# Kernel optimization log

Measured on AMD Instinct MI355X. Metric: run time of the kernel, lower is better.

The kernel has to match this reference:

```python
import jax, jax.numpy as jnp
import numpy as np

H1, H2 = 32, 16


def _gru_layer(x, W_ih, W_hh, b_ih, b_hh, H):
    # x: [B, T, I]; W_ih: [3H, I]; W_hh: [3H, H]; biases: [3H]
    # PyTorch gate order: r, z, n
    B = x.shape[0]
    xW = jnp.einsum('bti,gi->btg', x, W_ih) + b_ih  # [B, T, 3H]

    def step(h, xw_t):
        gh = h @ W_hh.T + b_hh                      # [B, 3H]
        r = jax.nn.sigmoid(xw_t[:, :H] + gh[:, :H])
        z = jax.nn.sigmoid(xw_t[:, H:2 * H] + gh[:, H:2 * H])
        n = jnp.tanh(xw_t[:, 2 * H:] + r * gh[:, 2 * H:])
        h_new = (1.0 - z) * n + z * h
        return h_new, h_new

    h0 = jnp.zeros((B, H), dtype=x.dtype)
    _, ys = jax.lax.scan(step, h0, jnp.swapaxes(xW, 0, 1))  # ys: [T, B, H]
    return jnp.swapaxes(ys, 0, 1)


def setup_inputs() -> dict:
    key = jax.random.key(0)
    ks = jax.random.split(key, 11)
    B, I, T, O = 4096, 8, 512, 1

    def u(k, shape, fan):
        s = 1.0 / np.sqrt(fan)
        return jax.random.uniform(k, shape, jnp.float32, -s, s)

    return {
        'input_seq': jax.random.normal(ks[0], (B, I, T), jnp.float32),
        'W_ih1': u(ks[1], (3 * H1, I), H1),
        'W_hh1': u(ks[2], (3 * H1, H1), H1),
        'b_ih1': u(ks[3], (3 * H1,), H1),
        'b_hh1': u(ks[4], (3 * H1,), H1),
        'W_ih2': u(ks[5], (3 * H2, H1), H2),
        'W_hh2': u(ks[6], (3 * H2, H2), H2),
        'b_ih2': u(ks[7], (3 * H2,), H2),
        'b_hh2': u(ks[8], (3 * H2,), H2),
        'W_lin': u(ks[9], (O, H2), H2),
        'b_lin': u(ks[10], (O,), H2),
    }


def reference(input_seq, W_ih1, W_hh1, b_ih1, b_hh1,
              W_ih2, W_hh2, b_ih2, b_hh2, W_lin, b_lin):
    x = jnp.transpose(input_seq, (0, 2, 1))          # [B, T, I]
    h1 = _gru_layer(x, W_ih1, W_hh1, b_ih1, b_hh1, H1)   # [B, T, 32]
    h2 = _gru_layer(h1, W_ih2, W_hh2, b_ih2, b_hh2, H2)  # [B, T, 16]
    out = h2[:, -1, :] @ W_lin.T + b_lin             # [B, O]
    return jnp.squeeze(out)                          # [B] when O == 1
```

## Files before the change

### kernel.cpp

```cpp
#include <hip/hip_runtime.h>

typedef __attribute__((ext_vector_type(4))) float    f32x4;
typedef __attribute__((ext_vector_type(4))) unsigned u32x4;
typedef __attribute__((ext_vector_type(8))) short    s16x8;

#define LOG2E 1.44269504088896340736f
__device__ __forceinline__ float fexp2(float x){ return __builtin_amdgcn_exp2f(x); }
__device__ __forceinline__ float frcp (float x){ return __builtin_amdgcn_rcpf(x); }
__device__ __forceinline__ float sigf (float x){ return frcp(1.0f + fexp2(-LOG2E*x)); }
__device__ __forceinline__ float tanh_(float x){ return 1.0f - 2.0f*frcp(1.0f + fexp2(2.0f*LOG2E*x)); }

__device__ __forceinline__ f32x4 mfma16(u32x4 a, u32x4 b, f32x4 c){
    return __builtin_amdgcn_mfma_f32_16x16x32_bf16(
        __builtin_bit_cast(s16x8, a), __builtin_bit_cast(s16x8, b), c, 0, 0, 0);
}

__device__ __forceinline__ unsigned rne_bf16(float f){
    unsigned u = __builtin_bit_cast(unsigned, f);
    return (u + 0x7fffu + ((u >> 16) & 1u)) >> 16;
}
__device__ __forceinline__ u32x4 packdup4(const float* p){
    u32x4 r;
    #pragma unroll
    for (int q = 0; q < 4; ++q) {
        unsigned w = rne_bf16(p[q]);
        r[q] = w | (w << 16);
    }
    return r;
}
__device__ __forceinline__ u32x4 packdup4_lo(const float* p){
    u32x4 r;
    #pragma unroll
    for (int q = 0; q < 4; ++q) {
        unsigned wh = rne_bf16(p[q]);
        float    wf = __builtin_bit_cast(float, wh << 16);
        unsigned wl = rne_bf16(p[q] - wf);
        r[q] = wl | (wl << 16);
    }
    return r;
}
__device__ __forceinline__ unsigned packsplit(float h){
    unsigned hu = __builtin_bit_cast(unsigned, h);
    unsigned hm = hu & 0xffff0000u;
    float rem = h - __builtin_bit_cast(float, hm);
    unsigned ru = __builtin_bit_cast(unsigned, rem);
    return (hm >> 16) | (ru & 0xffff0000u);
}

__global__ __launch_bounds__(192)
void gru2_mfma(const float* __restrict__ x_g,
               const float* __restrict__ Wih1, const float* __restrict__ Whh1,
               const float* __restrict__ bih1, const float* __restrict__ bhh1,
               const float* __restrict__ Wih2, const float* __restrict__ Whh2,
               const float* __restrict__ bih2, const float* __restrict__ bhh2,
               const float* __restrict__ Wlin, const float* __restrict__ blin,
               float* __restrict__ out)
{
    const int tid = threadIdx.x;
    const int wid = tid / 64;
    const int l   = tid & 63;
    const int sl  = l & 15;
    const int g   = l >> 4;
    const int b0  = blockIdx.x * 16;

    __shared__ unsigned xpk[32][16][12];
    __shared__ unsigned h1b[2][16][36];
    __shared__ unsigned zl[4];

    {
        unsigned* p1 = &h1b[0][0][0];
        for (int k = tid; k < 2*16*36; k += 192) p1[k] = 0u;
        if (tid < 4) zl[tid] = 0u;
    }

    u32x4 fR0,fR0l, fR1,fR1l, fR2,fR2l, fZ0,fZ0l, fZ1,fZ1l, fZ2,fZ2l,
          fX0,fX0l, fA,fAl, fB,fBl;
    f32x4 cbR, cbZ, cbX, cbH;
    const u32x4 zero4 = {0u,0u,0u,0u};

    if (wid < 2) {
        const int Ub = wid * 16;
        const int gr = Ub + sl, gz = 32 + Ub + sl, gn = 64 + Ub + sl;
        fR0  = (g < 2) ? packdup4   (Wih1 + gr*8 + 4*g) : zero4;
        fR0l = (g < 2) ? packdup4_lo(Wih1 + gr*8 + 4*g) : zero4;
        fR1  = packdup4   (Whh1 + gr*32 + 4*g);
        fR1l = packdup4_lo(Whh1 + gr*32 + 4*g);
        fR2  = packdup4   (Whh1 + gr*32 + 16 + 4*g);
        fR2l = packdup4_lo(Whh1 + gr*32 + 16 + 4*g);
        fZ0  = (g < 2) ? packdup4   (Wih1 + gz*8 + 4*g) : zero4;
        fZ0l = (g < 2) ? packdup4_lo(Wih1 + gz*8 + 4*g) : zero4;
        fZ1  = packdup4   (Whh1 + gz*32 + 4*g);
        fZ1l = packdup4_lo(Whh1 + gz*32 + 4*g);
        fZ2  = packdup4   (Whh1 + gz*32 + 16 + 4*g);
        fZ2l = packdup4_lo(Whh1 + gz*32 + 16 + 4*g);
        fX0  = (g < 2) ? packdup4   (Wih1 + gn*8 + 4*g) : zero4;
        fX0l = (g < 2) ? packdup4_lo(Wih1 + gn*8 + 4*g) : zero4;
        fA   = packdup4   (Whh1 + gn*32 + 4*g);
        fAl  = packdup4_lo(Whh1 + gn*32 + 4*g);
        fB   = packdup4   (Whh1 + gn*32 + 16 + 4*g);
        fBl  = packdup4_lo(Whh1 + gn*32 + 16 + 4*g);
        #pragma unroll
        for (int e = 0; e < 4; ++e) {
            const int u = Ub + 4*g + e;
            cbR[e] = bih1[u]      + bhh1[u];
            cbZ[e] = bih1[32+u]   + bhh1[32+u];
            cbX[e] = bih1[64+u];
            cbH[e] = bhh1[64+u];
        }
    } else {
        fR0  = packdup4   (Wih2 + sl*32 + 4*g);
        fR0l = packdup4_lo(Wih2 + sl*32 + 4*g);
        fR1  = packdup4   (Wih2 + sl*32 + 16 + 4*g);
        fR1l = packdup4_lo(Wih2 + sl*32 + 16 + 4*g);
        fR2  = packdup4   (Whh2 + sl*16 + 4*g);
        fR2l = packdup4_lo(Whh2 + sl*16 + 4*g);
        fZ0  = packdup4   (Wih2 + (16+sl)*32 + 4*g);
        fZ0l = packdup4_lo(Wih2 + (16+sl)*32 + 4*g);
        fZ1  = packdup4   (Wih2 + (16+sl)*32 + 16 + 4*g);
        fZ1l = packdup4_lo(Wih2 + (16+sl)*32 + 16 + 4*g);
        fZ2  = packdup4   (Whh2 + (16+sl)*16 + 4*g);
        fZ2l = packdup4_lo(Whh2 + (16+sl)*16 + 4*g);
        fX0  = packdup4   (Wih2 + (32+sl)*32 + 4*g);
        fX0l = packdup4_lo(Wih2 + (32+sl)*32 + 4*g);
        fA   = packdup4   (Wih2 + (32+sl)*32 + 16 + 4*g);
        fAl  = packdup4_lo(Wih2 + (32+sl)*32 + 16 + 4*g);
        fB   = packdup4   (Whh2 + (32+sl)*16 + 4*g);
        fBl  = packdup4_lo(Whh2 + (32+sl)*16 + 4*g);
        #pragma unroll
        for (int e = 0; e < 4; ++e) {
            const int u = 4*g + e;
            cbR[e] = bih2[u]    + bhh2[u];
            cbZ[e] = bih2[16+u] + bhh2[16+u];
            cbX[e] = bih2[32+u];
            cbH[e] = bhh2[32+u];
        }
    }

    float hv[4] = {0.f,0.f,0.f,0.f};
    u32x4 own   = {0u,0u,0u,0u};
    const f32x4 zc = {0.f,0.f,0.f,0.f};

    #pragma unroll 1
    for (int i = 0; i <= 512; ++i) {
        if ((i & 31) == 0 && i < 512) {
            if (tid < 128) {
                const int s  = tid >> 3;
                const int ii = tid & 7;
                const float* xg = x_g + ((size_t)(b0 + s))*4096 + ii*512 + i;
                #pragma unroll
                for (int w4 = 0; w4 < 8; ++w4) {
                    const f32x4 v = *(const f32x4*)(xg + 4*w4);
                    #pragma unroll
                    for (int e = 0; e < 4; ++e)
                        xpk[w4*4 + e][s][ii] = packsplit(v[e]);
                }
            }
            __syncthreads();
        }

        const int pr = (i + 1) & 1;

        if (wid < 2 && i < 512) {
            const int tt = i & 31;
            const u32x4 bT0 = (g < 2) ? *(const u32x4*)&xpk[tt][sl][4*g]
                                      : *(const u32x4*)&zl[0];
            u32x4 bT1, bT2;
            if (wid == 0) { bT1 = own;
                            bT2 = *(const u32x4*)&h1b[pr][sl][16 + 4*g]; }
            else          { bT1 = *(const u32x4*)&h1b[pr][sl][4*g];
                            bT2 = own; }
            f32x4 crh, crl, czh, czl, cx, cnh, cnl;
            crh = mfma16(fR0,  bT0, cbR); crh = mfma16(fR1,  bT1, crh); crh = mfma16(fR2,  bT2, crh);
            crl = mfma16(fR0l, bT0, zc ); crl = mfma16(fR1l, bT1, crl); crl = mfma16(fR2l, bT2, crl);
            czh = mfma16(fZ0,  bT0, cbZ); czh = mfma16(fZ1,  bT1, czh); czh = mfma16(fZ2,  bT2, czh);
            czl = mfma16(fZ0l, bT0, zc ); czl = mfma16(fZ1l, bT1, czl); czl = mfma16(fZ2l, bT2, czl);
            cx  = mfma16(fX0,  bT0, cbX); cx  = mfma16(fX0l, bT0, cx );
            cnh = mfma16(fA,   bT1, cbH); cnh = mfma16(fB,   bT2, cnh);
            cnl = mfma16(fAl,  bT1, zc ); cnl = mfma16(fBl,  bT2, cnl);
            #pragma unroll
            for (int e = 0; e < 4; ++e) {
                const float r = sigf(crh[e] + crl[e]);
                const float z = sigf(czh[e] + czl[e]);
                const float n = tanh_(fmaf(r, cnh[e] + cnl[e], cx[e]));
                const float h = n + z*(hv[e] - n);
                hv[e] = h;
                own[e] = packsplit(h);
            }
            *(u32x4*)&h1b[i & 1][sl][(wid ? 16 : 0) + 4*g] = own;
        }

        if (wid == 2 && i > 0) {
            const u32x4 bU0 = *(const u32x4*)&h1b[pr][sl][4*g];
            const u32x4 bU1 = *(const u32x4*)&h1b[pr][sl][16 + 4*g];
            const u32x4 bU2 = own;
            f32x4 crh, crl, czh, czl, cx, cn;
            crh = mfma16(fR0,  bU0, cbR); crh = mfma16(fR1,  bU1, crh); crh = mfma16(fR2,  bU2, crh);
            crl = mfma16(fR0l, bU0, zc ); crl = mfma16(fR1l, bU1, crl); crl = mfma16(fR2l, bU2, crl);
            czh = mfma16(fZ0,  bU0, cbZ); czh = mfma16(fZ1,  bU1, czh); czh = mfma16(fZ2,  bU2, czh);
            czl = mfma16(fZ0l, bU0, zc ); czl = mfma16(fZ1l, bU1, czl); czl = mfma16(fZ2l, bU2, czl);
            cx  = mfma16(fX0,  bU0, cbX); cx  = mfma16(fA,   bU1, cx );
            cx  = mfma16(fX0l, bU0, cx ); cx  = mfma16(fAl,  bU1, cx );
            cn  = mfma16(fB,   bU2, cbH); cn  = mfma16(fBl,  bU2, cn );
            #pragma unroll
            for (int e = 0; e < 4; ++e) {
                const float r = sigf(crh[e] + crl[e]);
                const float z = sigf(czh[e] + czl[e]);
                const float n = tanh_(fmaf(r, cn[e], cx[e]));
                const float h = n + z*(hv[e] - n);
                hv[e] = h;
                own[e] = packsplit(h);
            }
        }

        __syncthreads();
    }

    if (wid == 2) {
        float acc = 0.0f;
        acc = fmaf(Wlin[4*g+0], hv[0], acc);
        acc = fmaf(Wlin[4*g+1], hv[1], acc);
        acc = fmaf(Wlin[4*g+2], hv[2], acc);
        acc = fmaf(Wlin[4*g+3], hv[3], acc);
        acc += __shfl_xor(acc, 16, 64);
        acc += __shfl_xor(acc, 32, 64);
        if (g == 0) out[b0 + sl] = acc + blin[0];
    }
}

extern "C" void kernel_launch(void* const* d_in, const int* in_sizes, int n_in,
                              void* d_out, int out_size, void* d_ws, size_t ws_size,
                              hipStream_t stream) {
    const float* x    = (const float*)d_in[0];
    const float* Wih1 = (const float*)d_in[1];
    const float* Whh1 = (const float*)d_in[2];
    const float* bih1 = (const float*)d_in[3];
    const float* bhh1 = (const float*)d_in[4];
    const float* Wih2 = (const float*)d_in[5];
    const float* Whh2 = (const float*)d_in[6];
    const float* bih2 = (const float*)d_in[7];
    const float* bhh2 = (const float*)d_in[8];
    const float* Wlin = (const float*)d_in[9];
    const float* blin = (const float*)d_in[10];
    float* out = (float*)d_out;

    dim3 grid(256), block(192);
    hipLaunchKernelGGL(gru2_mfma, grid, block, 0, stream,
                       x, Wih1, Whh1, bih1, bhh1, Wih2, Whh2, bih2, bhh2,
                       Wlin, blin, out);
}
```

Measured before the change: 311.6 us.

## Merge both GRU layers into a single wavefront and drop block barriers

The block shrinks from three wavefronts (two for layer 1, one for layer 2) to one wavefront that computes both layer-1 halves and then layer 2 each timestep. All weight fragments stay in registers, the hidden state is passed in registers, the h1 ping-pong LDS buffer goes away, and the per-step __syncthreads are removed. The next timestep's x fragment is also prefetched from LDS one step ahead. In exchange, all MFMAs run on one SIMD, so layer 2 now follows layer 1 serially inside each step instead of being pipelined across waves, and register pressure rises sharply.

```diff
diff --git a/kernel.cpp b/kernel.cpp
--- a/kernel.cpp
+++ b/kernel.cpp
@@ -22,10 +22,7 @@
 __device__ __forceinline__ u32x4 packdup4(const float* p){
     u32x4 r;
     #pragma unroll
-    for (int q = 0; q < 4; ++q) {
-        unsigned w = rne_bf16(p[q]);
-        r[q] = w | (w << 16);
-    }
+    for (int q = 0; q < 4; ++q) { unsigned w = rne_bf16(p[q]); r[q] = w | (w << 16); }
     return r;
 }
 __device__ __forceinline__ u32x4 packdup4_lo(const float* p){
@@ -47,7 +44,7 @@
     return (hm >> 16) | (ru & 0xffff0000u);
 }
 
-__global__ __launch_bounds__(192)
+__global__ __launch_bounds__(64, 1)
 void gru2_mfma(const float* __restrict__ x_g,
                const float* __restrict__ Wih1, const float* __restrict__ Whh1,
                const float* __restrict__ bih1, const float* __restrict__ bhh1,
@@ -56,171 +53,179 @@
                const float* __restrict__ Wlin, const float* __restrict__ blin,
                float* __restrict__ out)
 {
-    const int tid = threadIdx.x;
-    const int wid = tid / 64;
-    const int l   = tid & 63;
-    const int sl  = l & 15;
-    const int g   = l >> 4;
-    const int b0  = blockIdx.x * 16;
+    const int l  = threadIdx.x;
+    const int sl = l & 15;
+    const int g  = l >> 4;
+    const int b0 = blockIdx.x * 16;
 
     __shared__ unsigned xpk[32][16][12];
-    __shared__ unsigned h1b[2][16][36];
-    __shared__ unsigned zl[4];
-
-    {
-        unsigned* p1 = &h1b[0][0][0];
-        for (int k = tid; k < 2*16*36; k += 192) p1[k] = 0u;
-        if (tid < 4) zl[tid] = 0u;
-    }
-
-    u32x4 fR0,fR0l, fR1,fR1l, fR2,fR2l, fZ0,fZ0l, fZ1,fZ1l, fZ2,fZ2l,
-          fX0,fX0l, fA,fAl, fB,fBl;
-    f32x4 cbR, cbZ, cbX, cbH;
+
     const u32x4 zero4 = {0u,0u,0u,0u};
-
-    if (wid < 2) {
-        const int Ub = wid * 16;
+    const f32x4 zc    = {0.f,0.f,0.f,0.f};
+
+    u32x4 f1[2][18];
+    f32x4 cb1[2][4];
+    #pragma unroll
+    for (int hf = 0; hf < 2; ++hf) {
+        const int Ub = hf * 16;
         const int gr = Ub + sl, gz = 32 + Ub + sl, gn = 64 + Ub + sl;
-        fR0  = (g < 2) ? packdup4   (Wih1 + gr*8 + 4*g) : zero4;
-        fR0l = (g < 2) ? packdup4_lo(Wih1 + gr*8 + 4*g) : zero4;
-        fR1  = packdup4   (Whh1 + gr*32 + 4*g);
-        fR1l = packdup4_lo(Whh1 + gr*32 + 4*g);
-        fR2  = packdup4   (Whh1 + gr*32 + 16 + 4*g);
-        fR2l = packdup4_lo(Whh1 + gr*32 + 16 + 4*g);
-        fZ0  = (g < 2) ? packdup4   (Wih1 + gz*8 + 4*g) : zero4;
-        fZ0l = (g < 2) ? packdup4_lo(Wih1 + gz*8 + 4*g) : zero4;
-        fZ1  = packdup4   (Whh1 + gz*32 + 4*g);
-        fZ1l = packdup4_lo(Whh1 + gz*32 + 4*g);
-        fZ2  = packdup4   (Whh1 + gz*32 + 16 + 4*g);
-        fZ2l = packdup4_lo(Whh1 + gz*32 + 16 + 4*g);
-        fX0  = (g < 2) ? packdup4   (Wih1 + gn*8 + 4*g) : zero4;
-        fX0l = (g < 2) ? packdup4_lo(Wih1 + gn*8 + 4*g) : zero4;
-        fA   = packdup4   (Whh1 + gn*32 + 4*g);
-        fAl  = packdup4_lo(Whh1 + gn*32 + 4*g);
-        fB   = packdup4   (Whh1 + gn*32 + 16 + 4*g);
-        fBl  = packdup4_lo(Whh1 + gn*32 + 16 + 4*g);
+        f1[hf][0]  = (g < 2) ? packdup4   (Wih1 + gr*8 + 4*g) : zero4;
+        f1[hf][1]  = (g < 2) ? packdup4_lo(Wih1 + gr*8 + 4*g) : zero4;
+        f1[hf][2]  = packdup4   (Whh1 + gr*32 + 4*g);
+        f1[hf][3]  = packdup4_lo(Whh1 + gr*32 + 4*g);
+        f1[hf][4]  = packdup4   (Whh1 + gr*32 + 16 + 4*g);
+        f1[hf][5]  = packdup4_lo(Whh1 + gr*32 + 16 + 4*g);
+        f1[hf][6]  = (g < 2) ? packdup4   (Wih1 + gz*8 + 4*g) : zero4;
+        f1[hf][7]  = (g < 2) ? packdup4_lo(Wih1 + gz*8 + 4*g) : zero4;
+        f1[hf][8]  = packdup4   (Whh1 + gz*32 + 4*g);
+        f1[hf][9]  = packdup4_lo(Whh1 + gz*32 + 4*g);
+        f1[hf][10] = packdup4   (Whh1 + gz*32 + 16 + 4*g);
+        f1[hf][11] = packdup4_lo(Whh1 + gz*32 + 16 + 4*g);
+        f1[hf][12] = (g < 2) ? packdup4   (Wih1 + gn*8 + 4*g) : zero4;
+        f1[hf][13] = (g < 2) ? packdup4_lo(Wih1 + gn*8 + 4*g) : zero4;
+        f1[hf][14] = packdup4   (Whh1 + gn*32 + 4*g);
+        f1[hf][15] = packdup4_lo(Whh1 + gn*32 + 4*g);
+        f1[hf][16] = packdup4   (Whh1 + gn*32 + 16 + 4*g);
+        f1[hf][17] = packdup4_lo(Whh1 + gn*32 + 16 + 4*g);
         #pragma unroll
         for (int e = 0; e < 4; ++e) {
             const int u = Ub + 4*g + e;
-            cbR[e] = bih1[u]      + bhh1[u];
-            cbZ[e] = bih1[32+u]   + bhh1[32+u];
-            cbX[e] = bih1[64+u];
-            cbH[e] = bhh1[64+u];
-        }
-    } else {
-        fR0  = packdup4   (Wih2 + sl*32 + 4*g);
-        fR0l = packdup4_lo(Wih2 + sl*32 + 4*g);
-        fR1  = packdup4   (Wih2 + sl*32 + 16 + 4*g);
-        fR1l = packdup4_lo(Wih2 + sl*32 + 16 + 4*g);
-        fR2  = packdup4   (Whh2 + sl*16 + 4*g);
-        fR2l = packdup4_lo(Whh2 + sl*16 + 4*g);
-        fZ0  = packdup4   (Wih2 + (16+sl)*32 + 4*g);
-        fZ0l = packdup4_lo(Wih2 + (16+sl)*32 + 4*g);
-        fZ1  = packdup4   (Wih2 + (16+sl)*32 + 16 + 4*g);
-        fZ1l = packdup4_lo(Wih2 + (16+sl)*32 + 16 + 4*g);
-        fZ2  = packdup4   (Whh2 + (16+sl)*16 + 4*g);
-        fZ2l = packdup4_lo(Whh2 + (16+sl)*16 + 4*g);
-        fX0  = packdup4   (Wih2 + (32+sl)*32 + 4*g);
-        fX0l = packdup4_lo(Wih2 + (32+sl)*32 + 4*g);
-        fA   = packdup4   (Wih2 + (32+sl)*32 + 16 + 4*g);
-        fAl  = packdup4_lo(Wih2 + (32+sl)*32 + 16 + 4*g);
-        fB   = packdup4   (Whh2 + (32+sl)*16 + 4*g);
-        fBl  = packdup4_lo(Whh2 + (32+sl)*16 + 4*g);
+            cb1[hf][0][e] = bih1[u]      + bhh1[u];
+            cb1[hf][1][e] = bih1[32+u]   + bhh1[32+u];
+            cb1[hf][2][e] = bih1[64+u];
+            cb1[hf][3][e] = bhh1[64+u];
+        }
+    }
+    u32x4 f2[18];
+    f32x4 cb2[4];
+    {
+        f2[0]  = packdup4   (Wih2 + sl*32 + 4*g);
+        f2[1]  = packdup4_lo(Wih2 + sl*32 + 4*g);
+        f2[2]  = packdup4   (Wih2 + sl*32 + 16 + 4*g);
+        f2[3]  = packdup4_lo(Wih2 + sl*32 + 16 + 4*g);
+        f2[4]  = packdup4   (Whh2 + sl*16 + 4*g);
+        f2[5]  = packdup4_lo(Whh2 + sl*16 + 4*g);
+        f2[6]  = packdup4   (Wih2 + (16+sl)*32 + 4*g);
+        f2[7]  = packdup4_lo(Wih2 + (16+sl)*32 + 4*g);
+        f2[8]  = packdup4   (Wih2 + (16+sl)*32 + 16 + 4*g);
+        f2[9]  = packdup4_lo(Wih2 + (16+sl)*32 + 16 + 4*g);
+        f2[10] = packdup4   (Whh2 + (16+sl)*16 + 4*g);
+        f2[11] = packdup4_lo(Whh2 + (16+sl)*16 + 4*g);
+        f2[12] = packdup4   (Wih2 + (32+sl)*32 + 4*g);
+        f2[13] = packdup4_lo(Wih2 + (32+sl)*32 + 4*g);
+        f2[14] = packdup4   (Wih2 + (32+sl)*32 + 16 + 4*g);
+        f2[15] = packdup4_lo(Wih2 + (32+sl)*32 + 16 + 4*g);
+        f2[16] = packdup4   (Whh2 + (32+sl)*16 + 4*g);
+        f2[17] = packdup4_lo(Whh2 + (32+sl)*16 + 4*g);
         #pragma unroll
         for (int e = 0; e < 4; ++e) {
             const int u = 4*g + e;
-            cbR[e] = bih2[u]    + bhh2[u];
-            cbZ[e] = bih2[16+u] + bhh2[16+u];
-            cbX[e] = bih2[32+u];
-            cbH[e] = bhh2[32+u];
-        }
-    }
-
-    float hv[4] = {0.f,0.f,0.f,0.f};
-    u32x4 own   = {0u,0u,0u,0u};
-    const f32x4 zc = {0.f,0.f,0.f,0.f};
+            cb2[0][e] = bih2[u]    + bhh2[u];
+            cb2[1][e] = bih2[16+u] + bhh2[16+u];
+            cb2[2][e] = bih2[32+u];
+            cb2[3][e] = bhh2[32+u];
+        }
+    }
+
+    float hv1[2][4] = {{0.f,0.f,0.f,0.f},{0.f,0.f,0.f,0.f}};
+    float hv2[4]    = {0.f,0.f,0.f,0.f};
+    u32x4 own1_0 = zero4, own1_1 = zero4, own2 = zero4;
+    u32x4 xnext  = zero4;
 
     #pragma unroll 1
-    for (int i = 0; i <= 512; ++i) {
-        if ((i & 31) == 0 && i < 512) {
-            if (tid < 128) {
-                const int s  = tid >> 3;
-                const int ii = tid & 7;
-                const float* xg = x_g + ((size_t)(b0 + s))*4096 + ii*512 + i;
+    for (int i = 0; i < 512; ++i) {
+        const int tt = i & 31;
+        if (tt == 0) {
+            #pragma unroll
+            for (int r = 0; r < 2; ++r) {
+                const int ii = 2*g + r;
+                const float* xg = x_g + (size_t)(b0 + sl)*4096 + ii*512 + i;
                 #pragma unroll
                 for (int w4 = 0; w4 < 8; ++w4) {
                     const f32x4 v = *(const f32x4*)(xg + 4*w4);
                     #pragma unroll
                     for (int e = 0; e < 4; ++e)
-                        xpk[w4*4 + e][s][ii] = packsplit(v[e]);
+                        xpk[w4*4 + e][sl][ii] = packsplit(v[e]);
                 }
             }
-            __syncthreads();
-        }
-
-        const int pr = (i + 1) & 1;
-
-        if (wid < 2 && i < 512) {
-            const int tt = i & 31;
-            const u32x4 bT0 = (g < 2) ? *(const u32x4*)&xpk[tt][sl][4*g]
-                                      : *(const u32x4*)&zl[0];
-            u32x4 bT1, bT2;
-            if (wid == 0) { bT1 = own;
-                            bT2 = *(const u32x4*)&h1b[pr][sl][16 + 4*g]; }
-            else          { bT1 = *(const u32x4*)&h1b[pr][sl][4*g];
-                            bT2 = own; }
-            f32x4 crh, crl, czh, czl, cx, cnh, cnl;
-            crh = mfma16(fR0,  bT0, cbR); crh = mfma16(fR1,  bT1, crh); crh = mfma16(fR2,  bT2, crh);
-            crl = mfma16(fR0l, bT0, zc ); crl = mfma16(fR1l, bT1, crl); crl = mfma16(fR2l, bT2, crl);
-            czh = mfma16(fZ0,  bT0, cbZ); czh = mfma16(fZ1,  bT1, czh); czh = mfma16(fZ2,  bT2, czh);
-            czl = mfma16(fZ0l, bT0, zc ); czl = mfma16(fZ1l, bT1, czl); czl = mfma16(fZ2l, bT2, czl);
-            cx  = mfma16(fX0,  bT0, cbX); cx  = mfma16(fX0l, bT0, cx );
-            cnh = mfma16(fA,   bT1, cbH); cnh = mfma16(fB,   bT2, cnh);
-            cnl = mfma16(fAl,  bT1, zc ); cnl = mfma16(fBl,  bT2, cnl);
+            if (g < 2) xnext = *(const u32x4*)&xpk[0][sl][4*g];
+        }
+        const u32x4 bT0 = xnext;
+        if (g < 2 && tt < 31) xnext = *(const u32x4*)&xpk[tt+1][sl][4*g];
+
+        f32x4 acc[2][7];
+        #pragma unroll
+        for (int hf = 0; hf < 2; ++hf) {
+            f32x4 crh = mfma16(f1[hf][2],  own1_0, cb1[hf][0]);
+            crh       = mfma16(f1[hf][4],  own1_1, crh);
+            crh       = mfma16(f1[hf][0],  bT0,    crh);
+            f32x4 crl = mfma16(f1[hf][3],  own1_0, zc);
+            crl       = mfma16(f1[hf][5],  own1_1, crl);
+            crl       = mfma16(f1[hf][1],  bT0,    crl);
+            f32x4 czh = mfma16(f1[hf][8],  own1_0, cb1[hf][1]);
+            czh       = mfma16(f1[hf][10], own1_1, czh);
+            czh       = mfma16(f1[hf][6],  bT0,    czh);
+            f32x4 czl = mfma16(f1[hf][9],  own1_0, zc);
+            czl       = mfma16(f1[hf][11], own1_1, czl);
+            czl       = mfma16(f1[hf][7],  bT0,    czl);
+            f32x4 cx  = mfma16(f1[hf][12], bT0,    cb1[hf][2]);
+            cx        = mfma16(f1[hf][13], bT0,    cx);
+            f32x4 cnh = mfma16(f1[hf][14], own1_0, cb1[hf][3]);
+            cnh       = mfma16(f1[hf][16], own1_1, cnh);
+            f32x4 cnl = mfma16(f1[hf][15], own1_0, zc);
+            cnl       = mfma16(f1[hf][17], own1_1, cnl);
+            acc[hf][0]=crh; acc[hf][1]=crl; acc[hf][2]=czh; acc[hf][3]=czl;
+            acc[hf][4]=cx;  acc[hf][5]=cnh; acc[hf][6]=cnl;
+        }
+        #pragma unroll
+        for (int hf = 0; hf < 2; ++hf) {
+            u32x4 ow;
             #pragma unroll
             for (int e = 0; e < 4; ++e) {
-                const float r = sigf(crh[e] + crl[e]);
-                const float z = sigf(czh[e] + czl[e]);
-                const float n = tanh_(fmaf(r, cnh[e] + cnl[e], cx[e]));
-                const float h = n + z*(hv[e] - n);
-                hv[e] = h;
-                own[e] = packsplit(h);
+                const float r = sigf(acc[hf][0][e] + acc[hf][1][e]);
+                const float z = sigf(acc[hf][2][e] + acc[hf][3][e]);
+                const float n = tanh_(fmaf(r, acc[hf][5][e] + acc[hf][6][e], acc[hf][4][e]));
+                const float h = n + z*(hv1[hf][e] - n);
+                hv1[hf][e] = h;
+                ow[e] = packsplit(h);
             }
-            *(u32x4*)&h1b[i & 1][sl][(wid ? 16 : 0) + 4*g] = own;
-        }
-
-        if (wid == 2 && i > 0) {
-            const u32x4 bU0 = *(const u32x4*)&h1b[pr][sl][4*g];
-            const u32x4 bU1 = *(const u32x4*)&h1b[pr][sl][16 + 4*g];
-            const u32x4 bU2 = own;
-            f32x4 crh, crl, czh, czl, cx, cn;
-            crh = mfma16(fR0,  bU0, cbR); crh = mfma16(fR1,  bU1, crh); crh = mfma16(fR2,  bU2, crh);
-            crl = mfma16(fR0l, bU0, zc ); crl = mfma16(fR1l, bU1, crl); crl = mfma16(fR2l, bU2, crl);
-            czh = mfma16(fZ0,  bU0, cbZ); czh = mfma16(fZ1,  bU1, czh); czh = mfma16(fZ2,  bU2, czh);
-            czl = mfma16(fZ0l, bU0, zc ); czl = mfma16(fZ1l, bU1, czl); czl = mfma16(fZ2l, bU2, czl);
-            cx  = mfma16(fX0,  bU0, cbX); cx  = mfma16(fA,   bU1, cx );
-            cx  = mfma16(fX0l, bU0, cx ); cx  = mfma16(fAl,  bU1, cx );
-            cn  = mfma16(fB,   bU2, cbH); cn  = mfma16(fBl,  bU2, cn );
+            if (hf == 0) own1_0 = ow; else own1_1 = ow;
+        }
+        {
+            f32x4 crh = mfma16(f2[0],  own1_0, cb2[0]);
+            crh       = mfma16(f2[2],  own1_1, crh);
+            crh       = mfma16(f2[4],  own2,   crh);
+            f32x4 crl = mfma16(f2[1],  own1_0, zc);
+            crl       = mfma16(f2[3],  own1_1, crl);
+            crl       = mfma16(f2[5],  own2,   crl);
+            f32x4 czh = mfma16(f2[6],  own1_0, cb2[1]);
+            czh       = mfma16(f2[8],  own1_1, czh);
+            czh       = mfma16(f2[10], own2,   czh);
+            f32x4 czl = mfma16(f2[7],  own1_0, zc);
+            czl       = mfma16(f2[9],  own1_1, czl);
+            czl       = mfma16(f2[11], own2,   czl);
+            f32x4 cx  = mfma16(f2[12], own1_0, cb2[2]);
+            cx        = mfma16(f2[14], own1_1, cx);
+            cx        = mfma16(f2[13], own1_0, cx);
+            cx        = mfma16(f2[15], own1_1, cx);
+            f32x4 cn  = mfma16(f2[16], own2,   cb2[3]);
+            cn        = mfma16(f2[17], own2,   cn);
             #pragma unroll
             for (int e = 0; e < 4; ++e) {
                 const float r = sigf(crh[e] + crl[e]);
                 const float z = sigf(czh[e] + czl[e]);
                 const float n = tanh_(fmaf(r, cn[e], cx[e]));
-                const float h = n + z*(hv[e] - n);
-                hv[e] = h;
-                own[e] = packsplit(h);
+                const float h = n + z*(hv2[e] - n);
+                hv2[e] = h;
+                own2[e] = packsplit(h);
             }
         }
-
-        __syncthreads();
-    }
-
-    if (wid == 2) {
+    }
+
+    {
         float acc = 0.0f;
-        acc = fmaf(Wlin[4*g+0], hv[0], acc);
-        acc = fmaf(Wlin[4*g+1], hv[1], acc);
-        acc = fmaf(Wlin[4*g+2], hv[2], acc);
-        acc = fmaf(Wlin[4*g+3], hv[3], acc);
+        #pragma unroll
+        for (int e = 0; e < 4; ++e) acc = fmaf(Wlin[4*g+e], hv2[e], acc);
         acc += __shfl_xor(acc, 16, 64);
         acc += __shfl_xor(acc, 32, 64);
         if (g == 0) out[b0 + sl] = acc + blin[0];
@@ -243,7 +248,7 @@
     const float* blin = (const float*)d_in[10];
     float* out = (float*)d_out;
 
-    dim3 grid(256), block(192);
+    dim3 grid(256), block(64);
     hipLaunchKernelGGL(gru2_mfma, grid, block, 0, stream,
                        x, Wih1, Whh1, bih1, bhh1, Wih2, Whh2, bih2, bhh2,
                        Wlin, blin, out);
```

Result: slower. 590.3 us (+89.4%).

## Halve batch per block to 8 sequences, doubling grid across CUs

Applied to the files above, without the earlier changes.

Each block now handles 8 batch rows instead of 16, and the grid grows from 256 to 512 blocks. The 16-column MFMA tiles are filled by duplicating the 8 rows (s8 = sl & 7), so half the matrix work is redundant. The aim is to spread the serial 512-step recurrence over more CUs on MI355X (256 CUs), so each CU runs two latency-bound blocks instead of one. It also prefetches the next timestep's x operand one step ahead and reorders layer-2 MFMAs so the operand from the wave's own state is consumed first.

```diff
diff --git a/kernel.cpp b/kernel.cpp
--- a/kernel.cpp
+++ b/kernel.cpp
@@ -22,10 +22,7 @@
 __device__ __forceinline__ u32x4 packdup4(const float* p){
     u32x4 r;
     #pragma unroll
-    for (int q = 0; q < 4; ++q) {
-        unsigned w = rne_bf16(p[q]);
-        r[q] = w | (w << 16);
-    }
+    for (int q = 0; q < 4; ++q) { unsigned w = rne_bf16(p[q]); r[q] = w | (w << 16); }
     return r;
 }
 __device__ __forceinline__ u32x4 packdup4_lo(const float* p){
@@ -47,7 +44,7 @@
     return (hm >> 16) | (ru & 0xffff0000u);
 }
 
-__global__ __launch_bounds__(192)
+__global__ __launch_bounds__(192, 1)
 void gru2_mfma(const float* __restrict__ x_g,
                const float* __restrict__ Wih1, const float* __restrict__ Whh1,
                const float* __restrict__ bih1, const float* __restrict__ bhh1,
@@ -60,23 +57,24 @@
     const int wid = tid / 64;
     const int l   = tid & 63;
     const int sl  = l & 15;
+    const int s8  = sl & 7;
     const int g   = l >> 4;
-    const int b0  = blockIdx.x * 16;
-
-    __shared__ unsigned xpk[32][16][12];
-    __shared__ unsigned h1b[2][16][36];
-    __shared__ unsigned zl[4];
+    const int b0  = blockIdx.x * 8;
+
+    __shared__ unsigned xpk[32][8][12];
+    __shared__ unsigned h1b[2][8][36];
 
     {
         unsigned* p1 = &h1b[0][0][0];
-        for (int k = tid; k < 2*16*36; k += 192) p1[k] = 0u;
-        if (tid < 4) zl[tid] = 0u;
-    }
+        for (int k = tid; k < 2*8*36; k += 192) p1[k] = 0u;
+    }
+
+    const u32x4 zero4 = {0u,0u,0u,0u};
+    const f32x4 zc    = {0.f,0.f,0.f,0.f};
 
     u32x4 fR0,fR0l, fR1,fR1l, fR2,fR2l, fZ0,fZ0l, fZ1,fZ1l, fZ2,fZ2l,
           fX0,fX0l, fA,fAl, fB,fBl;
     f32x4 cbR, cbZ, cbX, cbH;
-    const u32x4 zero4 = {0u,0u,0u,0u};
 
     if (wid < 2) {
         const int Ub = wid * 16;
@@ -137,37 +135,40 @@
     }
 
     float hv[4] = {0.f,0.f,0.f,0.f};
-    u32x4 own   = {0u,0u,0u,0u};
-    const f32x4 zc = {0.f,0.f,0.f,0.f};
+    u32x4 own   = zero4;
+    u32x4 xnext = zero4;
 
     #pragma unroll 1
     for (int i = 0; i <= 512; ++i) {
-        if ((i & 31) == 0 && i < 512) {
+        const int tt = i & 31;
+        if (tt == 0 && i < 512) {
             if (tid < 128) {
-                const int s  = tid >> 3;
-                const int ii = tid & 7;
-                const float* xg = x_g + ((size_t)(b0 + s))*4096 + ii*512 + i;
+                const int s   = tid >> 4;
+                const int rem = tid & 15;
+                const int ii  = rem >> 1;
+                const int hf  = rem & 1;
+                const float* xg = x_g + ((size_t)(b0 + s))*4096 + ii*512 + i + hf*16;
                 #pragma unroll
-                for (int w4 = 0; w4 < 8; ++w4) {
-                    const f32x4 v = *(const f32x4*)(xg + 4*w4);
+                for (int q = 0; q < 4; ++q) {
+                    const f32x4 v = *(const f32x4*)(xg + 4*q);
                     #pragma unroll
                     for (int e = 0; e < 4; ++e)
-                        xpk[w4*4 + e][s][ii] = packsplit(v[e]);
+                        xpk[hf*16 + 4*q + e][s][ii] = packsplit(v[e]);
                 }
             }
             __syncthreads();
+            if (wid < 2 && g < 2) xnext = *(const u32x4*)&xpk[0][s8][4*g];
         }
 
         const int pr = (i + 1) & 1;
 
         if (wid < 2 && i < 512) {
-            const int tt = i & 31;
-            const u32x4 bT0 = (g < 2) ? *(const u32x4*)&xpk[tt][sl][4*g]
-                                      : *(const u32x4*)&zl[0];
+            const u32x4 bT0 = xnext;
+            if (g < 2 && tt < 31) xnext = *(const u32x4*)&xpk[tt+1][s8][4*g];
             u32x4 bT1, bT2;
             if (wid == 0) { bT1 = own;
-                            bT2 = *(const u32x4*)&h1b[pr][sl][16 + 4*g]; }
-            else          { bT1 = *(const u32x4*)&h1b[pr][sl][4*g];
+                            bT2 = *(const u32x4*)&h1b[pr][s8][16 + 4*g]; }
+            else          { bT1 = *(const u32x4*)&h1b[pr][s8][4*g];
                             bT2 = own; }
             f32x4 crh, crl, czh, czl, cx, cnh, cnl;
             crh = mfma16(fR0,  bT0, cbR); crh = mfma16(fR1,  bT1, crh); crh = mfma16(fR2,  bT2, crh);
@@ -186,21 +187,22 @@
                 hv[e] = h;
                 own[e] = packsplit(h);
             }
-            *(u32x4*)&h1b[i & 1][sl][(wid ? 16 : 0) + 4*g] = own;
+            if (sl < 8)
+                *(u32x4*)&h1b[i & 1][sl][(wid ? 16 : 0) + 4*g] = own;
         }
 
         if (wid == 2 && i > 0) {
-            const u32x4 bU0 = *(const u32x4*)&h1b[pr][sl][4*g];
-            const u32x4 bU1 = *(const u32x4*)&h1b[pr][sl][16 + 4*g];
+            const u32x4 bU0 = *(const u32x4*)&h1b[pr][s8][4*g];
+            const u32x4 bU1 = *(const u32x4*)&h1b[pr][s8][16 + 4*g];
             const u32x4 bU2 = own;
             f32x4 crh, crl, czh, czl, cx, cn;
-            crh = mfma16(fR0,  bU0, cbR); crh = mfma16(fR1,  bU1, crh); crh = mfma16(fR2,  bU2, crh);
-            crl = mfma16(fR0l, bU0, zc ); crl = mfma16(fR1l, bU1, crl); crl = mfma16(fR2l, bU2, crl);
-            czh = mfma16(fZ0,  bU0, cbZ); czh = mfma16(fZ1,  bU1, czh); czh = mfma16(fZ2,  bU2, czh);
-            czl = mfma16(fZ0l, bU0, zc ); czl = mfma16(fZ1l, bU1, czl); czl = mfma16(fZ2l, bU2, czl);
+            crh = mfma16(fR2,  bU2, cbR); crh = mfma16(fR0,  bU0, crh); crh = mfma16(fR1,  bU1, crh);
+            crl = mfma16(fR2l, bU2, zc ); crl = mfma16(fR0l, bU0, crl); crl = mfma16(fR1l, bU1, crl);
+            czh = mfma16(fZ2,  bU2, cbZ); czh = mfma16(fZ0,  bU0, czh); czh = mfma16(fZ1,  bU1, czh);
+            czl = mfma16(fZ2l, bU2, zc ); czl = mfma16(fZ0l, bU0, czl); czl = mfma16(fZ1l, bU1, czl);
+            cn  = mfma16(fB,   bU2, cbH); cn  = mfma16(fBl,  bU2, cn );
             cx  = mfma16(fX0,  bU0, cbX); cx  = mfma16(fA,   bU1, cx );
             cx  = mfma16(fX0l, bU0, cx ); cx  = mfma16(fAl,  bU1, cx );
-            cn  = mfma16(fB,   bU2, cbH); cn  = mfma16(fBl,  bU2, cn );
             #pragma unroll
             for (int e = 0; e < 4; ++e) {
                 const float r = sigf(crh[e] + crl[e]);
@@ -223,7 +225,7 @@
         acc = fmaf(Wlin[4*g+3], hv[3], acc);
         acc += __shfl_xor(acc, 16, 64);
         acc += __shfl_xor(acc, 32, 64);
-        if (g == 0) out[b0 + sl] = acc + blin[0];
+        if (g == 0 && sl < 8) out[b0 + sl] = acc + blin[0];
     }
 }
 
@@ -243,7 +245,7 @@
     const float* blin = (const float*)d_in[10];
     float* out = (float*)d_out;
 
-    dim3 grid(256), block(192);
+    dim3 grid(512), block(192);
     hipLaunchKernelGGL(gru2_mfma, grid, block, 0, stream,
                        x, Wih1, Whh1, bih1, bhh1, Wih2, Whh2, bih2, bhh2,
                        Wlin, blin, out);
```

Result: slower. 450.5 us (+44.6%).
